# Kernel optimization log

Measured on AMD Instinct MI355X. Metric: run time of the kernel, lower is better.

Reference implementation:

```python
import jax, jax.numpy as jnp
import numpy as np

N_ENTITY = 100000
N_RELATION = 32
DIM = 64
N_LAYER = 2
B = 4096
T = 32


def _knowledge_attention(h_set, path, t_emb, W1, W2):
    # h_set, path, t_emb: [B, T, D]
    x = jnp.concatenate([h_set, path], axis=-1)          # [B, T, 2D]
    a = jax.nn.sigmoid(jax.nn.sigmoid(x @ W1) @ W2)      # [B, T]
    w = jax.nn.softmax(a, axis=-1)                       # softmax over triples
    return jnp.einsum('bt,btd->bd', w, t_emb)            # [B, D]


def _branch(h_idx, r_idx, t_idx, ent, rel, W1, W2):
    # h_idx/r_idx/t_idx: [L, B, T] ints. Faithful to the original loop,
    # which re-adds layer-i head emb and re-multiplies layer-i relation emb i times.
    outs = []
    for i in range(N_LAYER):
        h_set = ent[h_idx[0]]                            # [B, T, D]
        path = rel[r_idx[0]]                             # [B, T, D]
        for _k in range(1, i + 1):
            h_set = h_set + ent[h_idx[i]]
            path = path * rel[r_idx[i]]
        outs.append(_knowledge_attention(h_set, path, ent[t_idx[i]], W1, W2))
    return outs


def setup_inputs() -> dict:
    key = jax.random.key(0)
    ks = jax.random.split(key, 20)
    d = {}
    d['items'] = jax.random.randint(ks[0], (B,), 0, N_ENTITY)
    names = ['uis', 'ipt', 'upt', 'iot']
    i = 1
    for nm in names:
        d[nm + '_h'] = jax.random.randint(ks[i], (N_LAYER, B, T), 0, N_ENTITY); i += 1
        d[nm + '_r'] = jax.random.randint(ks[i], (N_LAYER, B, T), 0, N_RELATION); i += 1
        d[nm + '_t'] = jax.random.randint(ks[i], (N_LAYER, B, T), 0, N_ENTITY); i += 1
    # xavier-ish scales
    d['ent_emb'] = jax.random.normal(ks[13], (N_ENTITY, DIM), jnp.float32) * 0.05
    d['rel_emb'] = jax.random.normal(ks[14], (N_RELATION, DIM), jnp.float32) * 0.05
    d['W1'] = jax.random.normal(ks[15], (2 * DIM, DIM), jnp.float32) * (1.0 / np.sqrt(2 * DIM))
    d['W2'] = jax.random.normal(ks[16], (DIM,), jnp.float32) * (1.0 / np.sqrt(DIM))
    return d


def reference(items, uis_h, uis_r, uis_t, ipt_h, ipt_r, ipt_t,
              upt_h, upt_r, upt_t, iot_h, iot_r, iot_t,
              ent_emb, rel_emb, W1, W2):
    # user embeddings (init triple set)
    user_embs = [ent_emb[uis_h[0]].mean(axis=1)]
    user_embs += _branch(uis_h, uis_r, uis_t, ent_emb, rel_emb, W1, W2)
    # item embeddings (potential triple set)
    item_embs = [ent_emb[items]]
    item_embs += _branch(ipt_h, ipt_r, ipt_t, ent_emb, rel_emb, W1, W2)
    # user potential embeddings
    upo_embs = [ent_emb[upt_h[0]].mean(axis=1)]
    upo_embs += _branch(upt_h, upt_r, upt_t, ent_emb, rel_emb, W1, W2)
    # item origin embeddings
    ior_embs = [ent_emb[iot_h[0]].mean(axis=1)]
    ior_embs += _branch(iot_h, iot_r, iot_t, ent_emb, rel_emb, W1, W2)
    # agg == 'sum': extra item term appended before predict
    item_embs.append(ent_emb[ipt_h[0]].mean(axis=1))
    e_u = sum(user_embs[1:], user_embs[0])
    e_i = sum(item_embs[1:], item_embs[0])
    e_p_u = sum(upo_embs[1:], upo_embs[0])
    e_p_i = sum(ior_embs[1:], ior_embs[0])
    e_u = jnp.concatenate([e_u, e_p_u], axis=-1)
    e_i = jnp.concatenate([e_p_i, e_i], axis=-1)
    scores = jax.nn.sigmoid((e_i * e_u).sum(axis=1))     # [B]
    kge_loss = jnp.float32(0.0)                          # agg='sum' path: no SSL loss
    return scores, kge_loss
```

## Files before the change

### kernel.cpp

```cpp
#include <hip/hip_runtime.h>


#define NE   100000
#define NR   32
#define DIMD 64
#define BB   4096
#define TT   32
#define BT   (BB * TT)

__device__ __forceinline__ float sigf(float x) { return 1.0f / (1.0f + __expf(-x)); }
__device__ __forceinline__ float4 ld4(const float* p) {
    return *reinterpret_cast<const float4*>(p);
}

template <int CTRL>
__device__ __forceinline__ float dpp_add(float x) {
    int r = __builtin_amdgcn_update_dpp(0, __builtin_bit_cast(int, x), CTRL,
                                        0xf, 0xf, true);
    return x + __builtin_bit_cast(float, r);
}
__device__ __forceinline__ float reduce16(float x) {
    x = dpp_add<0x121>(x);
    x = dpp_add<0x122>(x);
    x = dpp_add<0x124>(x);
    x = dpp_add<0x128>(x);
    return x;
}

__global__ __launch_bounds__(256) void k_proj_ent(const float* __restrict__ ent,
                                                  const float* __restrict__ W1,
                                                  float* __restrict__ outP,
                                                  int pshift,
                                                  float* __restrict__ outE,
                                                  int eshift) {
    __shared__ float sW[64][68];
    __shared__ float sR[64][68];
    const int tid = threadIdx.x;
    const int row0 = blockIdx.x * 64;

#pragma unroll
    for (int i = 0; i < 4; ++i) {
        const int idx = tid + 256 * i;
        const int r = idx >> 4;
        const int c = idx & 15;
        const float4 wv = ld4(W1 + r * DIMD + 4 * c);
        sW[r][4 * c + 0] = wv.x; sW[r][4 * c + 1] = wv.y;
        sW[r][4 * c + 2] = wv.z; sW[r][4 * c + 3] = wv.w;
        const int er = (row0 + r < NE) ? (row0 + r) : (NE - 1);
        const float4 rv = ld4(ent + er * DIMD + 4 * c);
        sR[r][4 * c + 0] = rv.x; sR[r][4 * c + 1] = rv.y;
        sR[r][4 * c + 2] = rv.z; sR[r][4 * c + 3] = rv.w;
    }
    __syncthreads();

    const int q = tid & 15;
    const int trow = tid >> 4;
    float4 acc0 = make_float4(0.f, 0.f, 0.f, 0.f);
    float4 acc1 = acc0, acc2 = acc0, acc3 = acc0;

#pragma unroll
    for (int kk = 0; kk < 16; ++kk) {
        const float4 r0 = ld4(&sR[4 * trow + 0][4 * kk]);
        const float4 r1 = ld4(&sR[4 * trow + 1][4 * kk]);
        const float4 r2 = ld4(&sR[4 * trow + 2][4 * kk]);
        const float4 r3 = ld4(&sR[4 * trow + 3][4 * kk]);
#pragma unroll
        for (int i = 0; i < 4; ++i) {
            const float4 wv = ld4(&sW[4 * kk + i][4 * q]);
            const float s0 = (i == 0) ? r0.x : (i == 1) ? r0.y : (i == 2) ? r0.z : r0.w;
            const float s1 = (i == 0) ? r1.x : (i == 1) ? r1.y : (i == 2) ? r1.z : r1.w;
            const float s2 = (i == 0) ? r2.x : (i == 1) ? r2.y : (i == 2) ? r2.z : r2.w;
            const float s3 = (i == 0) ? r3.x : (i == 1) ? r3.y : (i == 2) ? r3.z : r3.w;
            acc0.x = fmaf(s0, wv.x, acc0.x); acc0.y = fmaf(s0, wv.y, acc0.y);
            acc0.z = fmaf(s0, wv.z, acc0.z); acc0.w = fmaf(s0, wv.w, acc0.w);
            acc1.x = fmaf(s1, wv.x, acc1.x); acc1.y = fmaf(s1, wv.y, acc1.y);
            acc1.z = fmaf(s1, wv.z, acc1.z); acc1.w = fmaf(s1, wv.w, acc1.w);
            acc2.x = fmaf(s2, wv.x, acc2.x); acc2.y = fmaf(s2, wv.y, acc2.y);
            acc2.z = fmaf(s2, wv.z, acc2.z); acc2.w = fmaf(s2, wv.w, acc2.w);
            acc3.x = fmaf(s3, wv.x, acc3.x); acc3.y = fmaf(s3, wv.y, acc3.y);
            acc3.z = fmaf(s3, wv.z, acc3.z); acc3.w = fmaf(s3, wv.w, acc3.w);
        }
    }

    const int orow = row0 + 4 * trow;
#pragma unroll
    for (int i = 0; i < 4; ++i) {
        if (orow + i < NE) {
            const float4 a = (i == 0) ? acc0 : (i == 1) ? acc1 : (i == 2) ? acc2 : acc3;
            *reinterpret_cast<float4*>(outP + ((size_t)(orow + i) << pshift) + 4 * q) = a;
            if (outE)
                *reinterpret_cast<float4*>(outE + ((size_t)(orow + i) << eshift) + 4 * q) =
                    ld4(&sR[4 * trow + i][4 * q]);
        }
    }
}

__global__ __launch_bounds__(256) void k_proj_rel(const float* __restrict__ rel,
                                                  const float* __restrict__ W1,
                                                  float* __restrict__ Prel1,
                                                  float* __restrict__ Prel2) {
    int gid = blockIdx.x * 256 + threadIdx.x;
    int row = gid >> 6;
    int d = gid & 63;
    if (row < 1024) {
        const float* a = rel + (row >> 5) * DIMD;
        const float* c = rel + (row & 31) * DIMD;
        float acc = 0.0f;
#pragma unroll
        for (int k = 0; k < DIMD; ++k)
            acc = fmaf(a[k] * c[k], W1[(DIMD + k) * DIMD + d], acc);
        Prel2[row * DIMD + d] = acc;
    } else if (row < 1056) {
        const float* a = rel + (row - 1024) * DIMD;
        float acc = 0.0f;
#pragma unroll
        for (int k = 0; k < DIMD; ++k)
            acc = fmaf(a[k], W1[(DIMD + k) * DIMD + d], acc);
        Prel1[(row - 1024) * DIMD + d] = acc;
    }
}

__global__ __launch_bounds__(256) void k_main(
    const int* __restrict__ items,
    const int* __restrict__ uh, const int* __restrict__ ur, const int* __restrict__ ut,
    const int* __restrict__ ih, const int* __restrict__ ir, const int* __restrict__ itp,
    const int* __restrict__ ph, const int* __restrict__ pr, const int* __restrict__ pt,
    const int* __restrict__ oh, const int* __restrict__ orr, const int* __restrict__ ot,
    const float* __restrict__ entT, int eshift,
    const float* __restrict__ pentT, int pshift,
    const float* __restrict__ W2,
    const float* __restrict__ Prel1, const float* __restrict__ Prel2,
    float* __restrict__ out) {
    const int b = blockIdx.x;
    const int tid = threadIdx.x;
    const int w = tid >> 6;
    const int lane = tid & 63;
    const int g = lane >> 4;
    const int q = lane & 15;

    const int* hp;
    const int* rp;
    const int* tp;
    switch (w) {
        case 0: hp = uh; rp = ur; tp = ut; break;
        case 1: hp = ih; rp = ir; tp = itp; break;
        case 2: hp = ph; rp = pr; tp = pt; break;
        default: hp = oh; rp = orr; tp = ot; break;
    }

    __shared__ int sidx[4][3][2][TT];
    {
        const int l = lane >> 5;
        const int t0 = lane & 31;
        const int off = l * BT + b * TT + t0;
        sidx[w][0][l][t0] = hp[off];
        sidx[w][1][l][t0] = rp[off];
        sidx[w][2][l][t0] = tp[off];
    }
    const int item_idx = (w == 1) ? items[b] : 0;

    const float4 w2v = ld4(W2 + 4 * q);

    float d0[8], d1[8];
    float4 accH = make_float4(0.f, 0.f, 0.f, 0.f);
#pragma unroll
    for (int p = 0; p < 8; ++p) {
        const int t = 4 * p + g;
        const int ih0 = sidx[w][0][0][t];
        const int ih1 = sidx[w][0][1][t];
        const int ir0 = sidx[w][1][0][t];
        const int ir1 = sidx[w][1][1][t];
        const float4 A0 = ld4(pentT + ((size_t)ih0 << pshift) + 4 * q);
        const float4 H  = ld4(entT + ((size_t)ih0 << eshift) + 4 * q);
        const float4 A1 = ld4(pentT + ((size_t)ih1 << pshift) + 4 * q);
        const float4 R0 = ld4(Prel1 + (ir0 << 6) + 4 * q);
        const float4 R2 = ld4(Prel2 + ((ir0 * 32 + ir1) << 6) + 4 * q);

        accH.x += H.x; accH.y += H.y; accH.z += H.z; accH.w += H.w;

        float v = sigf(A0.x + R0.x) * w2v.x;
        v = fmaf(sigf(A0.y + R0.y), w2v.y, v);
        v = fmaf(sigf(A0.z + R0.z), w2v.z, v);
        v = fmaf(sigf(A0.w + R0.w), w2v.w, v);
        d0[p] = v;

        float u = sigf(A0.x + A1.x + R2.x) * w2v.x;
        u = fmaf(sigf(A0.y + A1.y + R2.y), w2v.y, u);
        u = fmaf(sigf(A0.z + A1.z + R2.z), w2v.z, u);
        u = fmaf(sigf(A0.w + A1.w + R2.w), w2v.w, u);
        d1[p] = u;
    }

    float e0[8], e1[8];
    float s0 = 0.0f, s1 = 0.0f;
#pragma unroll
    for (int p = 0; p < 8; ++p) {
        e0[p] = __expf(sigf(reduce16(d0[p])));
        e1[p] = __expf(sigf(reduce16(d1[p])));
        s0 += e0[p];
        s1 += e1[p];
    }
    s0 += __shfl_xor(s0, 16, 64);
    s0 += __shfl_xor(s0, 32, 64);
    s1 += __shfl_xor(s1, 16, 64);
    s1 += __shfl_xor(s1, 32, 64);

    float4 acc0 = make_float4(0.f, 0.f, 0.f, 0.f);
    float4 acc1 = acc0;
#pragma unroll
    for (int p = 0; p < 8; ++p) {
        const int t = 4 * p + g;
        const int it0 = sidx[w][2][0][t];
        const int it1 = sidx[w][2][1][t];
        const float4 T0 = ld4(entT + ((size_t)it0 << eshift) + 4 * q);
        const float4 T1 = ld4(entT + ((size_t)it1 << eshift) + 4 * q);
        acc0.x = fmaf(e0[p], T0.x, acc0.x); acc0.y = fmaf(e0[p], T0.y, acc0.y);
        acc0.z = fmaf(e0[p], T0.z, acc0.z); acc0.w = fmaf(e0[p], T0.w, acc0.w);
        acc1.x = fmaf(e1[p], T1.x, acc1.x); acc1.y = fmaf(e1[p], T1.y, acc1.y);
        acc1.z = fmaf(e1[p], T1.z, acc1.z); acc1.w = fmaf(e1[p], T1.w, acc1.w);
    }

    const float inv0 = 1.0f / s0;
    const float inv1 = 1.0f / s1;
    float4 v;
    v.x = fmaf(acc0.x, inv0, fmaf(acc1.x, inv1, 0.03125f * accH.x));
    v.y = fmaf(acc0.y, inv0, fmaf(acc1.y, inv1, 0.03125f * accH.y));
    v.z = fmaf(acc0.z, inv0, fmaf(acc1.z, inv1, 0.03125f * accH.z));
    v.w = fmaf(acc0.w, inv0, fmaf(acc1.w, inv1, 0.03125f * accH.w));

    v.x += __shfl_xor(v.x, 16, 64); v.x += __shfl_xor(v.x, 32, 64);
    v.y += __shfl_xor(v.y, 16, 64); v.y += __shfl_xor(v.y, 32, 64);
    v.z += __shfl_xor(v.z, 16, 64); v.z += __shfl_xor(v.z, 32, 64);
    v.w += __shfl_xor(v.w, 16, 64); v.w += __shfl_xor(v.w, 32, 64);

    if (w == 1) {
        const float4 iv = ld4(entT + ((size_t)item_idx << eshift) + 4 * q);
        v.x += iv.x; v.y += iv.y; v.z += iv.z; v.w += iv.w;
    }

    __shared__ float vec[4][DIMD];
    if (g == 0) {
        vec[w][4 * q + 0] = v.x;
        vec[w][4 * q + 1] = v.y;
        vec[w][4 * q + 2] = v.z;
        vec[w][4 * q + 3] = v.w;
    }
    __syncthreads();

    if (tid < 64) {
        float z = fmaf(vec[0][tid], vec[3][tid], vec[2][tid] * vec[1][tid]);
#pragma unroll
        for (int m = 1; m < 64; m <<= 1) z += __shfl_xor(z, m, 64);
        if (tid == 0) out[b] = sigf(z);
    }
    if (b == 0 && tid == 0) out[BB] = 0.0f;
}

extern "C" void kernel_launch(void* const* d_in, const int* in_sizes, int n_in,
                              void* d_out, int out_size, void* d_ws, size_t ws_size,
                              hipStream_t stream) {
    const int* items = (const int*)d_in[0];
    const int* uh = (const int*)d_in[1];
    const int* ur = (const int*)d_in[2];
    const int* ut = (const int*)d_in[3];
    const int* ih = (const int*)d_in[4];
    const int* ir = (const int*)d_in[5];
    const int* itp = (const int*)d_in[6];
    const int* ph = (const int*)d_in[7];
    const int* pr = (const int*)d_in[8];
    const int* pt = (const int*)d_in[9];
    const int* oh = (const int*)d_in[10];
    const int* orr = (const int*)d_in[11];
    const int* ot = (const int*)d_in[12];
    const float* ent = (const float*)d_in[13];
    const float* rel = (const float*)d_in[14];
    const float* W1 = (const float*)d_in[15];
    const float* W2 = (const float*)d_in[16];
    float* out = (float*)d_out;

    float* Prel1 = (float*)d_ws;
    float* Prel2 = Prel1 + NR * DIMD;
    float* Ptab = Prel2 + 1024 * DIMD;

    const size_t head = (size_t)(NR * DIMD + 1024 * DIMD) * 4;
    const size_t need_merged = head + (size_t)NE * 128 * 4;
    const bool merged = ws_size >= need_merged;

    const float* entT;
    int eshift;
    float* pentT;
    int pshift;
    if (merged) {
        entT = Ptab;  eshift = 7;
        pentT = Ptab + 64; pshift = 7;
    } else {
        entT = ent;   eshift = 6;
        pentT = Ptab; pshift = 6;
    }

    hipLaunchKernelGGL(k_proj_ent, dim3((NE + 63) / 64), dim3(256), 0, stream,
                       ent, W1, pentT, pshift, merged ? (float*)entT : nullptr,
                       eshift);
    hipLaunchKernelGGL(k_proj_rel, dim3((1056 * 64 + 255) / 256), dim3(256), 0,
                       stream, rel, W1, Prel1, Prel2);
    hipLaunchKernelGGL(k_main, dim3(BB), dim3(256), 0, stream, items, uh, ur, ut,
                       ih, ir, itp, ph, pr, pt, oh, orr, ot, entT, eshift, pentT,
                       pshift, W2, Prel1, Prel2, out);
}
```

Before: 226.8 us.

## Fuse entity and relation projections into one kernel, drop interleaved table

Merges the relation projection into the entity projection kernel by giving the relation rows their own extra blocks that reuse the tiled shared-memory GEMM, which removes one kernel launch and replaces the naive per-thread relation dot-products. It also removes the interleaved [entity | projected-entity] 128-wide table. The main kernel now gathers raw embeddings from the original table and projected rows from a separate 64-wide table, so each gather row splits into two separate 256-byte fetches instead of one contiguous 512-byte fetch. In exchange the projection kernel writes half as much data.

After: 388.5 us. 1.71x slower.

```diff
diff --git a/kernel.cpp b/kernel.cpp
--- a/kernel.cpp
+++ b/kernel.cpp
@@ -8,9 +8,15 @@
 #define TT   32
 #define BT   (BB * TT)
 
+#define ENT_BLOCKS 1563
+#define REL_BLOCKS 17
+
 __device__ __forceinline__ float sigf(float x) { return 1.0f / (1.0f + __expf(-x)); }
 __device__ __forceinline__ float4 ld4(const float* p) {
     return *reinterpret_cast<const float4*>(p);
+}
+__device__ __forceinline__ void st4(float* p, float4 v) {
+    *reinterpret_cast<float4*>(p) = v;
 }
 
 template <int CTRL>
@@ -27,27 +33,42 @@
     return x;
 }
 
-__global__ __launch_bounds__(256) void k_proj_ent(const float* __restrict__ ent,
-                                                  const float* __restrict__ W1,
-                                                  float* __restrict__ outP,
-                                                  int pshift,
-                                                  float* __restrict__ outE,
-                                                  int eshift) {
+__global__ __launch_bounds__(256) void k_proj(const float* __restrict__ ent,
+                                              const float* __restrict__ rel,
+                                              const float* __restrict__ W1,
+                                              float* __restrict__ Pent,
+                                              float* __restrict__ Prel1,
+                                              float* __restrict__ Prel2) {
     __shared__ float sW[64][68];
     __shared__ float sR[64][68];
     const int tid = threadIdx.x;
-    const int row0 = blockIdx.x * 64;
+    const bool isEnt = blockIdx.x < ENT_BLOCKS;
+    const int base = isEnt ? blockIdx.x * 64 : (blockIdx.x - ENT_BLOCKS) * 64;
 
 #pragma unroll
     for (int i = 0; i < 4; ++i) {
         const int idx = tid + 256 * i;
         const int r = idx >> 4;
         const int c = idx & 15;
-        const float4 wv = ld4(W1 + r * DIMD + 4 * c);
+        const int wrow = isEnt ? r : (DIMD + r);
+        const float4 wv = ld4(W1 + wrow * DIMD + 4 * c);
         sW[r][4 * c + 0] = wv.x; sW[r][4 * c + 1] = wv.y;
         sW[r][4 * c + 2] = wv.z; sW[r][4 * c + 3] = wv.w;
-        const int er = (row0 + r < NE) ? (row0 + r) : (NE - 1);
-        const float4 rv = ld4(ent + er * DIMD + 4 * c);
+        float4 rv;
+        if (isEnt) {
+            const int er = (base + r < NE) ? (base + r) : (NE - 1);
+            rv = ld4(ent + er * DIMD + 4 * c);
+        } else {
+            const int ro = base + r;
+            if (ro < 1024) {
+                const float4 a = ld4(rel + (ro >> 5) * DIMD + 4 * c);
+                const float4 b = ld4(rel + (ro & 31) * DIMD + 4 * c);
+                rv = make_float4(a.x * b.x, a.y * b.y, a.z * b.z, a.w * b.w);
+            } else {
+                const int rr = (ro < 1056) ? (ro - 1024) : 0;
+                rv = ld4(rel + rr * DIMD + 4 * c);
+            }
+        }
         sR[r][4 * c + 0] = rv.x; sR[r][4 * c + 1] = rv.y;
         sR[r][4 * c + 2] = rv.z; sR[r][4 * c + 3] = rv.w;
     }
@@ -82,41 +103,16 @@
         }
     }
 
-    const int orow = row0 + 4 * trow;
 #pragma unroll
     for (int i = 0; i < 4; ++i) {
-        if (orow + i < NE) {
-            const float4 a = (i == 0) ? acc0 : (i == 1) ? acc1 : (i == 2) ? acc2 : acc3;
-            *reinterpret_cast<float4*>(outP + ((size_t)(orow + i) << pshift) + 4 * q) = a;
-            if (outE)
-                *reinterpret_cast<float4*>(outE + ((size_t)(orow + i) << eshift) + 4 * q) =
-                    ld4(&sR[4 * trow + i][4 * q]);
+        const float4 a = (i == 0) ? acc0 : (i == 1) ? acc1 : (i == 2) ? acc2 : acc3;
+        const int ro = base + 4 * trow + i;
+        if (isEnt) {
+            if (ro < NE) st4(Pent + (size_t)ro * DIMD + 4 * q, a);
+        } else {
+            if (ro < 1024) st4(Prel2 + ro * DIMD + 4 * q, a);
+            else if (ro < 1056) st4(Prel1 + (ro - 1024) * DIMD + 4 * q, a);
         }
-    }
-}
-
-__global__ __launch_bounds__(256) void k_proj_rel(const float* __restrict__ rel,
-                                                  const float* __restrict__ W1,
-                                                  float* __restrict__ Prel1,
-                                                  float* __restrict__ Prel2) {
-    int gid = blockIdx.x * 256 + threadIdx.x;
-    int row = gid >> 6;
-    int d = gid & 63;
-    if (row < 1024) {
-        const float* a = rel + (row >> 5) * DIMD;
-        const float* c = rel + (row & 31) * DIMD;
-        float acc = 0.0f;
-#pragma unroll
-        for (int k = 0; k < DIMD; ++k)
-            acc = fmaf(a[k] * c[k], W1[(DIMD + k) * DIMD + d], acc);
-        Prel2[row * DIMD + d] = acc;
-    } else if (row < 1056) {
-        const float* a = rel + (row - 1024) * DIMD;
-        float acc = 0.0f;
-#pragma unroll
-        for (int k = 0; k < DIMD; ++k)
-            acc = fmaf(a[k], W1[(DIMD + k) * DIMD + d], acc);
-        Prel1[(row - 1024) * DIMD + d] = acc;
     }
 }
 
@@ -280,30 +276,11 @@
 
     float* Prel1 = (float*)d_ws;
     float* Prel2 = Prel1 + NR * DIMD;
-    float* Ptab = Prel2 + 1024 * DIMD;
-
-    const size_t head = (size_t)(NR * DIMD + 1024 * DIMD) * 4;
-    const size_t need_merged = head + (size_t)NE * 128 * 4;
-    const bool merged = ws_size >= need_merged;
-
-    const float* entT;
-    int eshift;
-    float* pentT;
-    int pshift;
-    if (merged) {
-        entT = Ptab;  eshift = 7;
-        pentT = Ptab + 64; pshift = 7;
-    } else {
-        entT = ent;   eshift = 6;
-        pentT = Ptab; pshift = 6;
-    }
-
-    hipLaunchKernelGGL(k_proj_ent, dim3((NE + 63) / 64), dim3(256), 0, stream,
-                       ent, W1, pentT, pshift, merged ? (float*)entT : nullptr,
-                       eshift);
-    hipLaunchKernelGGL(k_proj_rel, dim3((1056 * 64 + 255) / 256), dim3(256), 0,
-                       stream, rel, W1, Prel1, Prel2);
+    float* Pent = Prel2 + 1024 * DIMD;
+
+    hipLaunchKernelGGL(k_proj, dim3(ENT_BLOCKS + REL_BLOCKS), dim3(256), 0,
+                       stream, ent, rel, W1, Pent, Prel1, Prel2);
     hipLaunchKernelGGL(k_main, dim3(BB), dim3(256), 0, stream, items, uh, ur, ut,
-                       ih, ir, itp, ph, pr, pt, oh, orr, ot, entT, eshift, pentT,
-                       pshift, W2, Prel1, Prel2, out);
-}
+                       ih, ir, itp, ph, pr, pt, oh, orr, ot, ent, 6, Pent, 6,
+                       W2, Prel1, Prel2, out);
+}
```
